# Optimization experiments

Hardware: AMD Instinct MI355X
Metric: run time of the kernel (lower is better)

Reference implementation:

```python
import jax, jax.numpy as jnp
import numpy as np

EPS = 1e-5

def _layer_norm(x, gamma, beta):
    m = jnp.mean(x, axis=-1, keepdims=True)
    v = jnp.mean(jnp.square(x - m), axis=-1, keepdims=True)
    return (x - m) * jax.lax.rsqrt(v + EPS) * gamma + beta

def setup_inputs() -> dict:
    key = jax.random.key(0)
    ks = jax.random.split(key, 6)
    B, D, H = 4096, 1024, 1024
    s = 1.0 / np.sqrt(H)
    return {
        "inputs": jax.random.normal(ks[0], (B, D), jnp.float32),
        "hx": jax.random.normal(ks[1], (B, H), jnp.float32),
        "cx": jax.random.normal(ks[2], (B, H), jnp.float32),
        "w_ih": jax.random.uniform(ks[3], (4 * H, D), jnp.float32, -s, s),
        "w_hh": jax.random.uniform(ks[4], (4 * H, H), jnp.float32, -s, s),
        "b_hh": jax.random.uniform(ks[5], (4 * H,), jnp.float32, -s, s),
        "g_ih": jnp.ones((4 * H,), jnp.float32),
        "beta_ih": jnp.zeros((4 * H,), jnp.float32),
        "g_hh": jnp.ones((4 * H,), jnp.float32),
        "beta_hh": jnp.zeros((4 * H,), jnp.float32),
        "g_ho": jnp.ones((H,), jnp.float32),
        "beta_ho": jnp.zeros((H,), jnp.float32),
    }

def reference(inputs, hx, cx, w_ih, w_hh, b_hh, g_ih, beta_ih, g_hh, beta_hh, g_ho, beta_ho):
    # i2h: [B, 4H] (no input bias used in original forward)
    i2h = inputs @ w_ih.T
    h2h = hx @ w_hh.T + b_hh
    gates = _layer_norm(i2h, g_ih, beta_ih) + _layer_norm(h2h, g_hh, beta_hh)
    i, f, o, g = jnp.split(gates, 4, axis=1)  # torch chunk order: i, f, o, g
    cy = jax.nn.sigmoid(f) * cx + jax.nn.sigmoid(i) * jnp.tanh(g)
    hy = jax.nn.sigmoid(o) * _layer_norm(jnp.tanh(cy), g_ho, beta_ho)
    # Dropout(0.1) is identity in eval / deterministic reference
    return hy, cy
```

## Files before the change

kernel.cpp:

```cpp
#include <hip/hip_runtime.h>
#include <hip/hip_bf16.h>
#include <stdint.h>

typedef __attribute__((ext_vector_type(8))) short bf16x8;
typedef __attribute__((ext_vector_type(4))) float f32x4;

#define LN_EPS 1e-5f

__device__ inline unsigned f2bf(float f) {
    unsigned u = __builtin_bit_cast(unsigned, f);
    u += 0x7fffu + ((u >> 16) & 1u);
    return u >> 16;
}
__device__ inline float bf2f(unsigned u) {
    return __builtin_bit_cast(float, u << 16);
}
__device__ inline float sigf(float x) {
    return 1.0f / (1.0f + __expf(-x));
}
__device__ inline float tanh_fast(float x) {
    return __builtin_fmaf(2.0f, 1.0f / (1.0f + __expf(-2.0f * x)), -1.0f);
}
__device__ inline float wred(float v) {
#pragma unroll
    for (int o = 32; o > 0; o >>= 1) v += __shfl_xor(v, o);
    return v;
}
__device__ inline void gload_lds16(const void* g, void* l) {
    __builtin_amdgcn_global_load_lds(
        (const __attribute__((address_space(1))) void*)g,
        (__attribute__((address_space(3))) void*)l, 16, 0, 0);
}

__global__ __launch_bounds__(256) void cast_all(
    const float4* __restrict__ s0, ushort4* __restrict__ d0, int n0,
    const float4* __restrict__ s1, ushort4* __restrict__ d1, int n1,
    const float4* __restrict__ s2, ushort4* __restrict__ d2, int n2,
    const float4* __restrict__ s3, ushort4* __restrict__ d3, int n3)
{
    int j = blockIdx.x * blockDim.x + threadIdx.x;
    const float4* s; ushort4* d;
    if (j < n0) { s = s0; d = d0; }
    else {
        j -= n0;
        if (j < n1) { s = s1; d = d1; }
        else {
            j -= n1;
            if (j < n2) { s = s2; d = d2; }
            else {
                j -= n2;
                if (j >= n3) return;
                s = s3; d = d3;
            }
        }
    }
    float4 v = s[j];
    ushort4 o;
    o.x = (unsigned short)f2bf(v.x); o.y = (unsigned short)f2bf(v.y);
    o.z = (unsigned short)f2bf(v.z); o.w = (unsigned short)f2bf(v.w);
    d[j] = o;
}

#define GNT 32

__global__ __launch_bounds__(512) void gemm8p(
    const short* __restrict__ Aa, const short* __restrict__ Ba, unsigned short* __restrict__ Ca,
    const short* __restrict__ Ab, const short* __restrict__ Bb, unsigned short* __restrict__ Cb,
    const float* __restrict__ Bias,
    float2* __restrict__ P,
    int N, int K)
{
    __shared__ __attribute__((aligned(16))) short lds[65536];
    short* ldsA = lds;
    short* ldsB = lds + 32768;

    const int gx  = gridDim.x;
    const int gxy = gx * gridDim.y;
    int bid = (blockIdx.z * gridDim.y + blockIdx.y) * gx + blockIdx.x;
    const int cpx = (gxy * gridDim.z) >> 3;
    int swz = (bid & 7) * cpx + (bid >> 3);
    const int z  = swz / gxy;
    const int r2 = swz - z * gxy;
    const int by = r2 / gx;
    const int bx = r2 - by * gx;

    const short* __restrict__ A = z ? Ab : Aa;
    const short* __restrict__ B = z ? Bb : Ba;
    unsigned short* __restrict__ C = z ? Cb : Ca;
    const int brow = by * 256, bcol = bx * 256;

    const int t    = threadIdx.x;
    const int lane = t & 63, w = t >> 6;
    const int wr = w >> 2, wc = w & 3;
    const int lr = lane & 15, kc = lane >> 4;

    const int ci0 = t, ci1 = t + 512;
    const int r0 = ci0 >> 2, l0 = (ci0 & 3) ^ ((r0 >> 1) & 3);
    const int r1 = ci1 >> 2, l1 = (ci1 & 3) ^ ((r1 >> 1) & 3);
    const int gA0 = (brow + r0) * K + l0 * 8;
    const int gA1 = (brow + r1) * K + l1 * 8;
    const int gB0 = (bcol + r0) * K + l0 * 8;
    const int gB1 = (bcol + r1) * K + l1 * 8;
    const int d0 = ci0 * 8, d1 = ci1 * 8;

#define STAGE_A(u) { const int so_ = ((u) & 3) * 8192; \
    gload_lds16(A + gA0 + (u) * 32, ldsA + so_ + d0);  \
    gload_lds16(A + gA1 + (u) * 32, ldsA + so_ + d1); }
#define STAGE_B(u) { const int so_ = ((u) & 3) * 8192; \
    gload_lds16(B + gB0 + (u) * 32, ldsB + so_ + d0);  \
    gload_lds16(B + gB1 + (u) * 32, ldsB + so_ + d1); }

    int offW[8], offX[4];
#pragma unroll
    for (int f = 0; f < 8; ++f) {
        int r = wr * 128 + f * 16 + lr;
        offW[f] = r * 32 + ((kc ^ ((r >> 1) & 3)) * 8);
    }
#pragma unroll
    for (int n = 0; n < 4; ++n) {
        int r = wc * 64 + n * 16 + lr;
        offX[n] = r * 32 + ((kc ^ ((r >> 1) & 3)) * 8);
    }

    f32x4 acc[8][4];
#pragma unroll
    for (int i = 0; i < 8; ++i)
#pragma unroll
        for (int j = 0; j < 4; ++j)
            acc[i][j] = (f32x4){0.f, 0.f, 0.f, 0.f};

    STAGE_A(0); STAGE_B(0); STAGE_A(1); STAGE_B(1); STAGE_A(2);
    asm volatile("s_waitcnt vmcnt(6)" ::: "memory");
    __builtin_amdgcn_s_barrier();

#pragma unroll 4
    for (int T = 0; T < GNT; ++T) {
        const int so = (T & 3) * 8192;
        bf16x8 w0, w1, w2, w3, x0, x1, x2, x3;

        w0 = *(const bf16x8*)&ldsB[so + offW[0]];
        w1 = *(const bf16x8*)&ldsB[so + offW[1]];
        w2 = *(const bf16x8*)&ldsB[so + offW[2]];
        w3 = *(const bf16x8*)&ldsB[so + offW[3]];
        x0 = *(const bf16x8*)&ldsA[so + offX[0]];
        x1 = *(const bf16x8*)&ldsA[so + offX[1]];
        x2 = *(const bf16x8*)&ldsA[so + offX[2]];
        x3 = *(const bf16x8*)&ldsA[so + offX[3]];
        if (T + 2 < GNT) STAGE_B(T + 2);
        __builtin_amdgcn_s_barrier();
        asm volatile("s_waitcnt lgkmcnt(0)" ::: "memory");
        __builtin_amdgcn_sched_barrier(0);
        __builtin_amdgcn_s_setprio(1);
        acc[0][0] = __builtin_amdgcn_mfma_f32_16x16x32_bf16(w0, x0, acc[0][0], 0, 0, 0);
        acc[0][1] = __builtin_amdgcn_mfma_f32_16x16x32_bf16(w0, x1, acc[0][1], 0, 0, 0);
        acc[0][2] = __builtin_amdgcn_mfma_f32_16x16x32_bf16(w0, x2, acc[0][2], 0, 0, 0);
        acc[0][3] = __builtin_amdgcn_mfma_f32_16x16x32_bf16(w0, x3, acc[0][3], 0, 0, 0);
        acc[1][0] = __builtin_amdgcn_mfma_f32_16x16x32_bf16(w1, x0, acc[1][0], 0, 0, 0);
        acc[1][1] = __builtin_amdgcn_mfma_f32_16x16x32_bf16(w1, x1, acc[1][1], 0, 0, 0);
        acc[1][2] = __builtin_amdgcn_mfma_f32_16x16x32_bf16(w1, x2, acc[1][2], 0, 0, 0);
        acc[1][3] = __builtin_amdgcn_mfma_f32_16x16x32_bf16(w1, x3, acc[1][3], 0, 0, 0);
        acc[2][0] = __builtin_amdgcn_mfma_f32_16x16x32_bf16(w2, x0, acc[2][0], 0, 0, 0);
        acc[2][1] = __builtin_amdgcn_mfma_f32_16x16x32_bf16(w2, x1, acc[2][1], 0, 0, 0);
        acc[2][2] = __builtin_amdgcn_mfma_f32_16x16x32_bf16(w2, x2, acc[2][2], 0, 0, 0);
        acc[2][3] = __builtin_amdgcn_mfma_f32_16x16x32_bf16(w2, x3, acc[2][3], 0, 0, 0);
        acc[3][0] = __builtin_amdgcn_mfma_f32_16x16x32_bf16(w3, x0, acc[3][0], 0, 0, 0);
        acc[3][1] = __builtin_amdgcn_mfma_f32_16x16x32_bf16(w3, x1, acc[3][1], 0, 0, 0);
        acc[3][2] = __builtin_amdgcn_mfma_f32_16x16x32_bf16(w3, x2, acc[3][2], 0, 0, 0);
        acc[3][3] = __builtin_amdgcn_mfma_f32_16x16x32_bf16(w3, x3, acc[3][3], 0, 0, 0);
        __builtin_amdgcn_s_setprio(0);
        __builtin_amdgcn_s_barrier();

        w0 = *(const bf16x8*)&ldsB[so + offW[4]];
        w1 = *(const bf16x8*)&ldsB[so + offW[5]];
        w2 = *(const bf16x8*)&ldsB[so + offW[6]];
        w3 = *(const bf16x8*)&ldsB[so + offW[7]];
        if (T + 3 < GNT) STAGE_A(T + 3);
        __builtin_amdgcn_s_barrier();
        asm volatile("s_waitcnt lgkmcnt(0)" ::: "memory");
        __builtin_amdgcn_sched_barrier(0);
        __builtin_amdgcn_s_setprio(1);
        acc[4][0] = __builtin_amdgcn_mfma_f32_16x16x32_bf16(w0, x0, acc[4][0], 0, 0, 0);
        acc[4][1] = __builtin_amdgcn_mfma_f32_16x16x32_bf16(w0, x1, acc[4][1], 0, 0, 0);
        acc[4][2] = __builtin_amdgcn_mfma_f32_16x16x32_bf16(w0, x2, acc[4][2], 0, 0, 0);
        acc[4][3] = __builtin_amdgcn_mfma_f32_16x16x32_bf16(w0, x3, acc[4][3], 0, 0, 0);
        acc[5][0] = __builtin_amdgcn_mfma_f32_16x16x32_bf16(w1, x0, acc[5][0], 0, 0, 0);
        acc[5][1] = __builtin_amdgcn_mfma_f32_16x16x32_bf16(w1, x1, acc[5][1], 0, 0, 0);
        acc[5][2] = __builtin_amdgcn_mfma_f32_16x16x32_bf16(w1, x2, acc[5][2], 0, 0, 0);
        acc[5][3] = __builtin_amdgcn_mfma_f32_16x16x32_bf16(w1, x3, acc[5][3], 0, 0, 0);
        acc[6][0] = __builtin_amdgcn_mfma_f32_16x16x32_bf16(w2, x0, acc[6][0], 0, 0, 0);
        acc[6][1] = __builtin_amdgcn_mfma_f32_16x16x32_bf16(w2, x1, acc[6][1], 0, 0, 0);
        acc[6][2] = __builtin_amdgcn_mfma_f32_16x16x32_bf16(w2, x2, acc[6][2], 0, 0, 0);
        acc[6][3] = __builtin_amdgcn_mfma_f32_16x16x32_bf16(w2, x3, acc[6][3], 0, 0, 0);
        acc[7][0] = __builtin_amdgcn_mfma_f32_16x16x32_bf16(w3, x0, acc[7][0], 0, 0, 0);
        acc[7][1] = __builtin_amdgcn_mfma_f32_16x16x32_bf16(w3, x1, acc[7][1], 0, 0, 0);
        acc[7][2] = __builtin_amdgcn_mfma_f32_16x16x32_bf16(w3, x2, acc[7][2], 0, 0, 0);
        acc[7][3] = __builtin_amdgcn_mfma_f32_16x16x32_bf16(w3, x3, acc[7][3], 0, 0, 0);
        __builtin_amdgcn_s_setprio(0);
        if (T < GNT - 3)      { asm volatile("s_waitcnt vmcnt(6)" ::: "memory"); }
        else if (T == GNT - 3){ asm volatile("s_waitcnt vmcnt(4)" ::: "memory"); }
        else if (T == GNT - 2){ asm volatile("s_waitcnt vmcnt(0)" ::: "memory"); }
        __builtin_amdgcn_s_barrier();
    }

    const int gc0   = bcol + wr * 128 + kc * 4;
    const int mrow0 = brow + wc * 64 + lr;

    float4 bias4[8];
#pragma unroll
    for (int f = 0; f < 8; ++f) {
        if (z) bias4[f] = *reinterpret_cast<const float4*>(&Bias[gc0 + f * 16]);
        else   bias4[f] = (float4){0.f, 0.f, 0.f, 0.f};
    }

    float s[4] = {0.f, 0.f, 0.f, 0.f}, q[4] = {0.f, 0.f, 0.f, 0.f};
#pragma unroll
    for (int f = 0; f < 8; ++f) {
#pragma unroll
        for (int n = 0; n < 4; ++n) {
            float v0 = acc[f][n][0] + bias4[f].x;
            float v1 = acc[f][n][1] + bias4[f].y;
            float v2 = acc[f][n][2] + bias4[f].z;
            float v3 = acc[f][n][3] + bias4[f].w;
            unsigned u0 = f2bf(v0), u1 = f2bf(v1), u2 = f2bf(v2), u3 = f2bf(v3);
            float e0 = bf2f(u0), e1 = bf2f(u1), e2 = bf2f(u2), e3 = bf2f(u3);
            s[n] += (e0 + e1) + (e2 + e3);
            q[n] += (e0 * e0 + e1 * e1) + (e2 * e2 + e3 * e3);
            uint2 pk; pk.x = u0 | (u1 << 16); pk.y = u2 | (u3 << 16);
            *reinterpret_cast<uint2*>(&C[(size_t)(mrow0 + n * 16) * N + gc0 + f * 16]) = pk;
        }
    }
#pragma unroll
    for (int n = 0; n < 4; ++n) {
        s[n] += __shfl_xor(s[n], 16); s[n] += __shfl_xor(s[n], 32);
        q[n] += __shfl_xor(q[n], 16); q[n] += __shfl_xor(q[n], 32);
    }

    __syncthreads();
    float2* part = (float2*)lds;
    if (kc == 0) {
#pragma unroll
        for (int n = 0; n < 4; ++n) {
            float2 pr; pr.x = s[n]; pr.y = q[n];
            part[wr * 256 + wc * 64 + n * 16 + lr] = pr;
        }
    }
    __syncthreads();
    if (t < 256) {
        float2 p0 = part[t], p1 = part[256 + t];
        float2 o; o.x = p0.x + p1.x; o.y = p0.y + p1.y;
        P[((size_t)(z * 16 + by) * 256 + t) * 16 + bx] = o;
    }
#undef STAGE_A
#undef STAGE_B
}

__global__ __launch_bounds__(256) void reduce_stats(const float2* __restrict__ P,
                                                    float2* __restrict__ stats, float invn) {
    const int row = blockIdx.x * 256 + threadIdx.x;
    float s = 0.f, q = 0.f;
#pragma unroll
    for (int b = 0; b < 16; ++b) { float2 v = P[(size_t)row * 16 + b]; s += v.x; q += v.y; }
    float m = s * invn;
    float r = rsqrtf(q * invn - m * m + LN_EPS);
    float2 o; o.x = m; o.y = r;
    stats[row] = o;
}

__global__ __launch_bounds__(256) void ln_lstm(
    const unsigned short* __restrict__ i2h,
    const unsigned short* __restrict__ h2h,
    const float* __restrict__ cx,
    const float2* __restrict__ statsI, const float2* __restrict__ statsH,
    const float* __restrict__ g_ih, const float* __restrict__ be_ih,
    const float* __restrict__ g_hh, const float* __restrict__ be_hh,
    const float* __restrict__ g_ho, const float* __restrict__ be_ho,
    float* __restrict__ hy, float* __restrict__ cy, int H)
{
    const int b = blockIdx.x;
    const int t = threadIdx.x;
    const int lane = t & 63;
    const int wave = t >> 6;
    const int H4 = 4 * H;
    const int h0 = t * 4;

    const unsigned short* xi = i2h + (size_t)b * H4;
    const unsigned short* xh = h2h + (size_t)b * H4;

    const float2 sI = statsI[b];
    const float2 sH = statsH[b];

    __shared__ float red[4][2];

    float gate[4][4];
#pragma unroll
    for (int q = 0; q < 4; ++q) {
        const int j = q * H + h0;
        ushort4 vi = *reinterpret_cast<const ushort4*>(&xi[j]);
        ushort4 vh = *reinterpret_cast<const ushort4*>(&xh[j]);
        float4 gi = *reinterpret_cast<const float4*>(&g_ih[j]);
        float4 bi = *reinterpret_cast<const float4*>(&be_ih[j]);
        float4 gh = *reinterpret_cast<const float4*>(&g_hh[j]);
        float4 bh = *reinterpret_cast<const float4*>(&be_hh[j]);
        gate[q][0] = (bf2f(vi.x) - sI.x) * sI.y * gi.x + bi.x + (bf2f(vh.x) - sH.x) * sH.y * gh.x + bh.x;
        gate[q][1] = (bf2f(vi.y) - sI.x) * sI.y * gi.y + bi.y + (bf2f(vh.y) - sH.x) * sH.y * gh.y + bh.y;
        gate[q][2] = (bf2f(vi.z) - sI.x) * sI.y * gi.z + bi.z + (bf2f(vh.z) - sH.x) * sH.y * gh.z + bh.z;
        gate[q][3] = (bf2f(vi.w) - sI.x) * sI.y * gi.w + bi.w + (bf2f(vh.w) - sH.x) * sH.y * gh.w + bh.w;
    }

    float4 cxv = *reinterpret_cast<const float4*>(&cx[(size_t)b * H + h0]);
    float cvals[4] = {cxv.x, cxv.y, cxv.z, cxv.w};
    float tv[4], ov[4];
    float s2 = 0.f, q2 = 0.f;
    float4 cyv;
#pragma unroll
    for (int k = 0; k < 4; ++k) {
        float c = sigf(gate[1][k]) * cvals[k] + sigf(gate[0][k]) * tanh_fast(gate[3][k]);
        ((float*)&cyv)[k] = c;
        float tc = tanh_fast(c);
        tv[k] = tc; ov[k] = sigf(gate[2][k]);
        s2 += tc; q2 += tc * tc;
    }
    *reinterpret_cast<float4*>(&cy[(size_t)b * H + h0]) = cyv;

    s2 = wred(s2); q2 = wred(q2);
    if (lane == 0) { red[wave][0] = s2; red[wave][1] = q2; }
    __syncthreads();
    float S2 = red[0][0] + red[1][0] + red[2][0] + red[3][0];
    float Q2 = red[0][1] + red[1][1] + red[2][1] + red[3][1];
    const float invH = 1.0f / (float)H;
    float mt = S2 * invH;
    float rt = rsqrtf(Q2 * invH - mt * mt + LN_EPS);

    float4 go = *reinterpret_cast<const float4*>(&g_ho[h0]);
    float4 bo = *reinterpret_cast<const float4*>(&be_ho[h0]);
    float4 hyv;
    hyv.x = ov[0] * ((tv[0] - mt) * rt * go.x + bo.x);
    hyv.y = ov[1] * ((tv[1] - mt) * rt * go.y + bo.y);
    hyv.z = ov[2] * ((tv[2] - mt) * rt * go.z + bo.z);
    hyv.w = ov[3] * ((tv[3] - mt) * rt * go.w + bo.w);
    *reinterpret_cast<float4*>(&hy[(size_t)b * H + h0]) = hyv;
}

extern "C" void kernel_launch(void* const* d_in, const int* in_sizes, int n_in,
                              void* d_out, int out_size, void* d_ws, size_t ws_size,
                              hipStream_t stream) {
    const float* inputs  = (const float*)d_in[0];
    const float* hx      = (const float*)d_in[1];
    const float* cx      = (const float*)d_in[2];
    const float* w_ih    = (const float*)d_in[3];
    const float* w_hh    = (const float*)d_in[4];
    const float* b_hh    = (const float*)d_in[5];
    const float* g_ih    = (const float*)d_in[6];
    const float* beta_ih = (const float*)d_in[7];
    const float* g_hh    = (const float*)d_in[8];
    const float* beta_hh = (const float*)d_in[9];
    const float* g_ho    = (const float*)d_in[10];
    const float* beta_ho = (const float*)d_in[11];

    const int H  = in_sizes[10];
    const int B  = in_sizes[1] / H;
    const int D  = in_sizes[0] / B;
    const int H4 = 4 * H;

    uint8_t* ws = (uint8_t*)d_ws;
    size_t off = 0;
    short* Abf  = (short*)(ws + off); off += (size_t)B * D * 2;
    short* Hbf  = (short*)(ws + off); off += (size_t)B * H * 2;
    short* Wih  = (short*)(ws + off); off += (size_t)H4 * D * 2;
    short* Whh  = (short*)(ws + off); off += (size_t)H4 * H * 2;
    unsigned short* i2hb = (unsigned short*)(ws + off); off += (size_t)B * H4 * 2;
    unsigned short* h2hb = (unsigned short*)(ws + off); off += (size_t)B * H4 * 2;
    float2* P     = (float2*)(ws + off); off += (size_t)2 * 16 * 256 * 16 * sizeof(float2);
    float2* stats = (float2*)(ws + off); off += (size_t)2 * B * sizeof(float2);

    float* hy  = (float*)d_out;
    float* cyo = (float*)d_out + (size_t)B * H;

    {
        const int n0 = (B * D) / 4, n1 = (B * H) / 4, n2 = (H4 * D) / 4, n3 = (H4 * H) / 4;
        const int tot = n0 + n1 + n2 + n3;
        cast_all<<<(tot + 255) / 256, 256, 0, stream>>>(
            (const float4*)inputs, (ushort4*)Abf, n0,
            (const float4*)hx,     (ushort4*)Hbf, n1,
            (const float4*)w_ih,   (ushort4*)Wih, n2,
            (const float4*)w_hh,   (ushort4*)Whh, n3);
    }

    {
        dim3 grid(H4 / 256, B / 256, 2);
        gemm8p<<<grid, 512, 0, stream>>>(Abf, Wih, i2hb, Hbf, Whh, h2hb, b_hh, P, H4, D);
    }

    reduce_stats<<<(2 * B) / 256, 256, 0, stream>>>(P, stats, 1.0f / (float)H4);

    ln_lstm<<<B, 256, 0, stream>>>(i2hb, h2hb, cx, stats, stats + B,
                                   g_ih, beta_ih, g_hh, beta_hh, g_ho, beta_ho,
                                   hy, cyo, H);
}
```

Baseline: 127.8 us.

## Stage GEMM output through LDS for coalesced stores and fold stats reduction into LSTM

The GEMM epilogue now keeps the packed bf16 results in registers, writes them into a swizzled LDS tile, and then stores full 16-byte rows to global memory instead of scattered 8-byte stores. The separate reduce_stats kernel is removed; ln_lstm now reduces the 16 per-block partial sums itself with a wave shuffle and computes mean and rstd in shared memory. This removes a kernel launch and improves store coalescing, at the cost of extra registers (pk[8][4]), an extra barrier in the GEMM, and a small serial prologue in every LSTM block.

```diff
diff --git a/kernel.cpp b/kernel.cpp
--- a/kernel.cpp
+++ b/kernel.cpp
@@ -202,16 +202,14 @@
         __builtin_amdgcn_s_barrier();
     }
 
-    const int gc0   = bcol + wr * 128 + kc * 4;
-    const int mrow0 = brow + wc * 64 + lr;
-
     float4 bias4[8];
 #pragma unroll
     for (int f = 0; f < 8; ++f) {
-        if (z) bias4[f] = *reinterpret_cast<const float4*>(&Bias[gc0 + f * 16]);
+        if (z) bias4[f] = *reinterpret_cast<const float4*>(&Bias[bcol + wr * 128 + f * 16 + kc * 4]);
         else   bias4[f] = (float4){0.f, 0.f, 0.f, 0.f};
     }
 
+    uint2 pk[8][4];
     float s[4] = {0.f, 0.f, 0.f, 0.f}, q[4] = {0.f, 0.f, 0.f, 0.f};
 #pragma unroll
     for (int f = 0; f < 8; ++f) {
@@ -225,8 +223,8 @@
             float e0 = bf2f(u0), e1 = bf2f(u1), e2 = bf2f(u2), e3 = bf2f(u3);
             s[n] += (e0 + e1) + (e2 + e3);
             q[n] += (e0 * e0 + e1 * e1) + (e2 * e2 + e3 * e3);
-            uint2 pk; pk.x = u0 | (u1 << 16); pk.y = u2 | (u3 << 16);
-            *reinterpret_cast<uint2*>(&C[(size_t)(mrow0 + n * 16) * N + gc0 + f * 16]) = pk;
+            pk[f][n].x = u0 | (u1 << 16);
+            pk[f][n].y = u2 | (u3 << 16);
         }
     }
 #pragma unroll
@@ -250,31 +248,43 @@
         float2 o; o.x = p0.x + p1.x; o.y = p0.y + p1.y;
         P[((size_t)(z * 16 + by) * 256 + t) * 16 + bx] = o;
     }
+    __syncthreads();
+
+    uint8_t* cb = (uint8_t*)lds;
+    const int rloc0 = wc * 64 + lr;
+#pragma unroll
+    for (int f = 0; f < 8; ++f) {
+        const int colB = wr * 256 + f * 32 + kc * 8;
+#pragma unroll
+        for (int n = 0; n < 4; ++n) {
+            const int r = rloc0 + n * 16;
+            *reinterpret_cast<uint2*>(cb + r * 512 + (colB ^ ((r & 7) << 4))) = pk[f][n];
+        }
+    }
+    __syncthreads();
+    {
+        const int rr = t >> 5;
+        const int cB = (t & 31) * 16;
+#pragma unroll
+        for (int i = 0; i < 16; ++i) {
+            const int r = rr + i * 16;
+            uint4 v = *reinterpret_cast<const uint4*>(cb + r * 512 + (cB ^ ((r & 7) << 4)));
+            *reinterpret_cast<uint4*>((uint8_t*)&C[(size_t)(brow + r) * N + bcol] + cB) = v;
+        }
+    }
 #undef STAGE_A
 #undef STAGE_B
-}
-
-__global__ __launch_bounds__(256) void reduce_stats(const float2* __restrict__ P,
-                                                    float2* __restrict__ stats, float invn) {
-    const int row = blockIdx.x * 256 + threadIdx.x;
-    float s = 0.f, q = 0.f;
-#pragma unroll
-    for (int b = 0; b < 16; ++b) { float2 v = P[(size_t)row * 16 + b]; s += v.x; q += v.y; }
-    float m = s * invn;
-    float r = rsqrtf(q * invn - m * m + LN_EPS);
-    float2 o; o.x = m; o.y = r;
-    stats[row] = o;
 }
 
 __global__ __launch_bounds__(256) void ln_lstm(
     const unsigned short* __restrict__ i2h,
     const unsigned short* __restrict__ h2h,
     const float* __restrict__ cx,
-    const float2* __restrict__ statsI, const float2* __restrict__ statsH,
+    const float2* __restrict__ P,
     const float* __restrict__ g_ih, const float* __restrict__ be_ih,
     const float* __restrict__ g_hh, const float* __restrict__ be_hh,
     const float* __restrict__ g_ho, const float* __restrict__ be_ho,
-    float* __restrict__ hy, float* __restrict__ cy, int H)
+    float* __restrict__ hy, float* __restrict__ cy, int H, int B)
 {
     const int b = blockIdx.x;
     const int t = threadIdx.x;
@@ -286,10 +296,27 @@
     const unsigned short* xi = i2h + (size_t)b * H4;
     const unsigned short* xh = h2h + (size_t)b * H4;
 
-    const float2 sI = statsI[b];
-    const float2 sH = statsH[b];
-
     __shared__ float red[4][2];
+    __shared__ float st[4];
+
+    if (wave == 0) {
+        const int half = (lane >> 4) & 1;
+        float2 v = (float2){0.f, 0.f};
+        if (lane < 32) v = P[((size_t)(half * B + b)) * 16 + (lane & 15)];
+        v.x += __shfl_xor(v.x, 1); v.y += __shfl_xor(v.y, 1);
+        v.x += __shfl_xor(v.x, 2); v.y += __shfl_xor(v.y, 2);
+        v.x += __shfl_xor(v.x, 4); v.y += __shfl_xor(v.y, 4);
+        v.x += __shfl_xor(v.x, 8); v.y += __shfl_xor(v.y, 8);
+        if (lane < 32 && (lane & 15) == 0) {
+            const float inv4H = 1.0f / (float)H4;
+            float m = v.x * inv4H;
+            float r = rsqrtf(v.y * inv4H - m * m + LN_EPS);
+            st[half * 2]     = m;
+            st[half * 2 + 1] = r;
+        }
+    }
+    __syncthreads();
+    const float mI = st[0], rI = st[1], mH = st[2], rH = st[3];
 
     float gate[4][4];
 #pragma unroll
@@ -301,10 +328,10 @@
         float4 bi = *reinterpret_cast<const float4*>(&be_ih[j]);
         float4 gh = *reinterpret_cast<const float4*>(&g_hh[j]);
         float4 bh = *reinterpret_cast<const float4*>(&be_hh[j]);
-        gate[q][0] = (bf2f(vi.x) - sI.x) * sI.y * gi.x + bi.x + (bf2f(vh.x) - sH.x) * sH.y * gh.x + bh.x;
-        gate[q][1] = (bf2f(vi.y) - sI.x) * sI.y * gi.y + bi.y + (bf2f(vh.y) - sH.x) * sH.y * gh.y + bh.y;
-        gate[q][2] = (bf2f(vi.z) - sI.x) * sI.y * gi.z + bi.z + (bf2f(vh.z) - sH.x) * sH.y * gh.z + bh.z;
-        gate[q][3] = (bf2f(vi.w) - sI.x) * sI.y * gi.w + bi.w + (bf2f(vh.w) - sH.x) * sH.y * gh.w + bh.w;
+        gate[q][0] = (bf2f(vi.x) - mI) * rI * gi.x + bi.x + (bf2f(vh.x) - mH) * rH * gh.x + bh.x;
+        gate[q][1] = (bf2f(vi.y) - mI) * rI * gi.y + bi.y + (bf2f(vh.y) - mH) * rH * gh.y + bh.y;
+        gate[q][2] = (bf2f(vi.z) - mI) * rI * gi.z + bi.z + (bf2f(vh.z) - mH) * rH * gh.z + bh.z;
+        gate[q][3] = (bf2f(vi.w) - mI) * rI * gi.w + bi.w + (bf2f(vh.w) - mH) * rH * gh.w + bh.w;
     }
 
     float4 cxv = *reinterpret_cast<const float4*>(&cx[(size_t)b * H + h0]);
@@ -370,8 +397,7 @@
     short* Whh  = (short*)(ws + off); off += (size_t)H4 * H * 2;
     unsigned short* i2hb = (unsigned short*)(ws + off); off += (size_t)B * H4 * 2;
     unsigned short* h2hb = (unsigned short*)(ws + off); off += (size_t)B * H4 * 2;
-    float2* P     = (float2*)(ws + off); off += (size_t)2 * 16 * 256 * 16 * sizeof(float2);
-    float2* stats = (float2*)(ws + off); off += (size_t)2 * B * sizeof(float2);
+    float2* P   = (float2*)(ws + off); off += (size_t)2 * B * 16 * sizeof(float2);
 
     float* hy  = (float*)d_out;
     float* cyo = (float*)d_out + (size_t)B * H;
@@ -391,9 +417,7 @@
         gemm8p<<<grid, 512, 0, stream>>>(Abf, Wih, i2hb, Hbf, Whh, h2hb, b_hh, P, H4, D);
     }
 
-    reduce_stats<<<(2 * B) / 256, 256, 0, stream>>>(P, stats, 1.0f / (float)H4);
-
-    ln_lstm<<<B, 256, 0, stream>>>(i2hb, h2hb, cx, stats, stats + B,
+    ln_lstm<<<B, 256, 0, stream>>>(i2hb, h2hb, cx, P,
                                    g_ih, beta_ih, g_hh, beta_hh, g_ho, beta_ho,
-                                   hy, cyo, H);
-}
+                                   hy, cyo, H, B);
+}
```

Result: no change. 126.5 us (-1.1%).

## Move layernorm row statistics from GEMM epilogue into the LSTM kernel

Applied to the files above, without the earlier changes.

The GEMM epilogue no longer adds the hidden bias or accumulates per-row sum and sum-of-squares partials, and the separate reduce_stats launch is removed. The ln_lstm kernel now adds b_hh itself and computes both layernorm statistics with a block reduction over the bf16 row values it already loads. This drops a kernel launch, the partial-stats traffic and the GEMM epilogue work and LDS syncs. In exchange it adds an extra block-wide reduction and barrier to ln_lstm, and the h2h row stats are now taken after bias is added to the bf16-rounded value rather than before rounding.

```diff
diff --git a/kernel.cpp b/kernel.cpp
--- a/kernel.cpp
+++ b/kernel.cpp
@@ -66,8 +66,6 @@
 __global__ __launch_bounds__(512) void gemm8p(
     const short* __restrict__ Aa, const short* __restrict__ Ba, unsigned short* __restrict__ Ca,
     const short* __restrict__ Ab, const short* __restrict__ Bb, unsigned short* __restrict__ Cb,
-    const float* __restrict__ Bias,
-    float2* __restrict__ P,
     int N, int K)
 {
     __shared__ __attribute__((aligned(16))) short lds[65536];
@@ -202,75 +200,27 @@
         __builtin_amdgcn_s_barrier();
     }
 
-    const int gc0   = bcol + wr * 128 + kc * 4;
-    const int mrow0 = brow + wc * 64 + lr;
-
-    float4 bias4[8];
+    const int gc0 = bcol + wr * 128 + kc * 4;
+    const int mr0 = brow + wc * 64 + lr;
 #pragma unroll
     for (int f = 0; f < 8; ++f) {
-        if (z) bias4[f] = *reinterpret_cast<const float4*>(&Bias[gc0 + f * 16]);
-        else   bias4[f] = (float4){0.f, 0.f, 0.f, 0.f};
-    }
-
-    float s[4] = {0.f, 0.f, 0.f, 0.f}, q[4] = {0.f, 0.f, 0.f, 0.f};
-#pragma unroll
-    for (int f = 0; f < 8; ++f) {
 #pragma unroll
         for (int n = 0; n < 4; ++n) {
-            float v0 = acc[f][n][0] + bias4[f].x;
-            float v1 = acc[f][n][1] + bias4[f].y;
-            float v2 = acc[f][n][2] + bias4[f].z;
-            float v3 = acc[f][n][3] + bias4[f].w;
-            unsigned u0 = f2bf(v0), u1 = f2bf(v1), u2 = f2bf(v2), u3 = f2bf(v3);
-            float e0 = bf2f(u0), e1 = bf2f(u1), e2 = bf2f(u2), e3 = bf2f(u3);
-            s[n] += (e0 + e1) + (e2 + e3);
-            q[n] += (e0 * e0 + e1 * e1) + (e2 * e2 + e3 * e3);
+            unsigned u0 = f2bf(acc[f][n][0]), u1 = f2bf(acc[f][n][1]);
+            unsigned u2 = f2bf(acc[f][n][2]), u3 = f2bf(acc[f][n][3]);
             uint2 pk; pk.x = u0 | (u1 << 16); pk.y = u2 | (u3 << 16);
-            *reinterpret_cast<uint2*>(&C[(size_t)(mrow0 + n * 16) * N + gc0 + f * 16]) = pk;
+            *reinterpret_cast<uint2*>(&C[(size_t)(mr0 + n * 16) * N + gc0 + f * 16]) = pk;
         }
-    }
-#pragma unroll
-    for (int n = 0; n < 4; ++n) {
-        s[n] += __shfl_xor(s[n], 16); s[n] += __shfl_xor(s[n], 32);
-        q[n] += __shfl_xor(q[n], 16); q[n] += __shfl_xor(q[n], 32);
-    }
-
-    __syncthreads();
-    float2* part = (float2*)lds;
-    if (kc == 0) {
-#pragma unroll
-        for (int n = 0; n < 4; ++n) {
-            float2 pr; pr.x = s[n]; pr.y = q[n];
-            part[wr * 256 + wc * 64 + n * 16 + lr] = pr;
-        }
-    }
-    __syncthreads();
-    if (t < 256) {
-        float2 p0 = part[t], p1 = part[256 + t];
-        float2 o; o.x = p0.x + p1.x; o.y = p0.y + p1.y;
-        P[((size_t)(z * 16 + by) * 256 + t) * 16 + bx] = o;
     }
 #undef STAGE_A
 #undef STAGE_B
-}
-
-__global__ __launch_bounds__(256) void reduce_stats(const float2* __restrict__ P,
-                                                    float2* __restrict__ stats, float invn) {
-    const int row = blockIdx.x * 256 + threadIdx.x;
-    float s = 0.f, q = 0.f;
-#pragma unroll
-    for (int b = 0; b < 16; ++b) { float2 v = P[(size_t)row * 16 + b]; s += v.x; q += v.y; }
-    float m = s * invn;
-    float r = rsqrtf(q * invn - m * m + LN_EPS);
-    float2 o; o.x = m; o.y = r;
-    stats[row] = o;
 }
 
 __global__ __launch_bounds__(256) void ln_lstm(
     const unsigned short* __restrict__ i2h,
     const unsigned short* __restrict__ h2h,
     const float* __restrict__ cx,
-    const float2* __restrict__ statsI, const float2* __restrict__ statsH,
+    const float* __restrict__ b_hh,
     const float* __restrict__ g_ih, const float* __restrict__ be_ih,
     const float* __restrict__ g_hh, const float* __restrict__ be_hh,
     const float* __restrict__ g_ho, const float* __restrict__ be_ho,
@@ -286,25 +236,51 @@
     const unsigned short* xi = i2h + (size_t)b * H4;
     const unsigned short* xh = h2h + (size_t)b * H4;
 
-    const float2 sI = statsI[b];
-    const float2 sH = statsH[b];
-
-    __shared__ float red[4][2];
-
-    float gate[4][4];
+    __shared__ float red[4][4];
+    __shared__ float red2[4][2];
+
+    float exi[4][4], exh[4][4];
+    float si = 0.f, qi = 0.f, sh = 0.f, qh = 0.f;
 #pragma unroll
     for (int q = 0; q < 4; ++q) {
         const int j = q * H + h0;
         ushort4 vi = *reinterpret_cast<const ushort4*>(&xi[j]);
         ushort4 vh = *reinterpret_cast<const ushort4*>(&xh[j]);
+        float4 bb = *reinterpret_cast<const float4*>(&b_hh[j]);
+        exi[q][0] = bf2f(vi.x); exi[q][1] = bf2f(vi.y);
+        exi[q][2] = bf2f(vi.z); exi[q][3] = bf2f(vi.w);
+        exh[q][0] = bf2f(vh.x) + bb.x; exh[q][1] = bf2f(vh.y) + bb.y;
+        exh[q][2] = bf2f(vh.z) + bb.z; exh[q][3] = bf2f(vh.w) + bb.w;
+#pragma unroll
+        for (int k = 0; k < 4; ++k) {
+            si += exi[q][k]; qi = __builtin_fmaf(exi[q][k], exi[q][k], qi);
+            sh += exh[q][k]; qh = __builtin_fmaf(exh[q][k], exh[q][k], qh);
+        }
+    }
+    si = wred(si); qi = wred(qi); sh = wred(sh); qh = wred(qh);
+    if (lane == 0) { red[wave][0] = si; red[wave][1] = qi; red[wave][2] = sh; red[wave][3] = qh; }
+    __syncthreads();
+    float Si = red[0][0] + red[1][0] + red[2][0] + red[3][0];
+    float Qi = red[0][1] + red[1][1] + red[2][1] + red[3][1];
+    float Sh = red[0][2] + red[1][2] + red[2][2] + red[3][2];
+    float Qh = red[0][3] + red[1][3] + red[2][3] + red[3][3];
+    const float inv4H = 1.0f / (float)H4;
+    const float mI = Si * inv4H, mH = Sh * inv4H;
+    const float rI = rsqrtf(Qi * inv4H - mI * mI + LN_EPS);
+    const float rH = rsqrtf(Qh * inv4H - mH * mH + LN_EPS);
+
+    float gate[4][4];
+#pragma unroll
+    for (int q = 0; q < 4; ++q) {
+        const int j = q * H + h0;
         float4 gi = *reinterpret_cast<const float4*>(&g_ih[j]);
         float4 bi = *reinterpret_cast<const float4*>(&be_ih[j]);
         float4 gh = *reinterpret_cast<const float4*>(&g_hh[j]);
         float4 bh = *reinterpret_cast<const float4*>(&be_hh[j]);
-        gate[q][0] = (bf2f(vi.x) - sI.x) * sI.y * gi.x + bi.x + (bf2f(vh.x) - sH.x) * sH.y * gh.x + bh.x;
-        gate[q][1] = (bf2f(vi.y) - sI.x) * sI.y * gi.y + bi.y + (bf2f(vh.y) - sH.x) * sH.y * gh.y + bh.y;
-        gate[q][2] = (bf2f(vi.z) - sI.x) * sI.y * gi.z + bi.z + (bf2f(vh.z) - sH.x) * sH.y * gh.z + bh.z;
-        gate[q][3] = (bf2f(vi.w) - sI.x) * sI.y * gi.w + bi.w + (bf2f(vh.w) - sH.x) * sH.y * gh.w + bh.w;
+        gate[q][0] = (exi[q][0] - mI) * rI * gi.x + bi.x + (exh[q][0] - mH) * rH * gh.x + bh.x;
+        gate[q][1] = (exi[q][1] - mI) * rI * gi.y + bi.y + (exh[q][1] - mH) * rH * gh.y + bh.y;
+        gate[q][2] = (exi[q][2] - mI) * rI * gi.z + bi.z + (exh[q][2] - mH) * rH * gh.z + bh.z;
+        gate[q][3] = (exi[q][3] - mI) * rI * gi.w + bi.w + (exh[q][3] - mH) * rH * gh.w + bh.w;
     }
 
     float4 cxv = *reinterpret_cast<const float4*>(&cx[(size_t)b * H + h0]);
@@ -323,10 +299,10 @@
     *reinterpret_cast<float4*>(&cy[(size_t)b * H + h0]) = cyv;
 
     s2 = wred(s2); q2 = wred(q2);
-    if (lane == 0) { red[wave][0] = s2; red[wave][1] = q2; }
+    if (lane == 0) { red2[wave][0] = s2; red2[wave][1] = q2; }
     __syncthreads();
-    float S2 = red[0][0] + red[1][0] + red[2][0] + red[3][0];
-    float Q2 = red[0][1] + red[1][1] + red[2][1] + red[3][1];
+    float S2 = red2[0][0] + red2[1][0] + red2[2][0] + red2[3][0];
+    float Q2 = red2[0][1] + red2[1][1] + red2[2][1] + red2[3][1];
     const float invH = 1.0f / (float)H;
     float mt = S2 * invH;
     float rt = rsqrtf(Q2 * invH - mt * mt + LN_EPS);
@@ -370,8 +346,6 @@
     short* Whh  = (short*)(ws + off); off += (size_t)H4 * H * 2;
     unsigned short* i2hb = (unsigned short*)(ws + off); off += (size_t)B * H4 * 2;
     unsigned short* h2hb = (unsigned short*)(ws + off); off += (size_t)B * H4 * 2;
-    float2* P     = (float2*)(ws + off); off += (size_t)2 * 16 * 256 * 16 * sizeof(float2);
-    float2* stats = (float2*)(ws + off); off += (size_t)2 * B * sizeof(float2);
 
     float* hy  = (float*)d_out;
     float* cyo = (float*)d_out + (size_t)B * H;
@@ -388,12 +362,10 @@
 
     {
         dim3 grid(H4 / 256, B / 256, 2);
-        gemm8p<<<grid, 512, 0, stream>>>(Abf, Wih, i2hb, Hbf, Whh, h2hb, b_hh, P, H4, D);
-    }
-
-    reduce_stats<<<(2 * B) / 256, 256, 0, stream>>>(P, stats, 1.0f / (float)H4);
-
-    ln_lstm<<<B, 256, 0, stream>>>(i2hb, h2hb, cx, stats, stats + B,
+        gemm8p<<<grid, 512, 0, stream>>>(Abf, Wih, i2hb, Hbf, Whh, h2hb, H4, D);
+    }
+
+    ln_lstm<<<B, 256, 0, stream>>>(i2hb, h2hb, cx, b_hh,
                                    g_ih, beta_ih, g_hh, beta_hh, g_ho, beta_ho,
                                    hy, cyo, H);
 }
```

Result: no change. 128.7 us (+0.7%).
